# Kernel optimization log

Hardware: AMD Instinct MI355X
Metric: run time of the kernel (lower is better)

The kernel has to match this reference:

```python
import jax, jax.numpy as jnp
import numpy as np

B, NX, NLQ = 2, 2048, 64
D_IN, D_OUT, H = 768, 768, 12
HD = D_OUT // H  # 64
P_X, P_LQ = 0.1, 0.2  # dropout probs for x-x block vs any learnable-query block
DROP_KEY = 42  # fixed key for dropout masks (training mode)


def setup_inputs() -> dict:
    key = jax.random.key(0)
    ks = jax.random.split(key, 6)
    s = 0.02
    return {
        "x": jax.random.normal(ks[0], (B, NX, D_IN), jnp.float32),
        "learnable_queries": jax.random.normal(ks[1], (B, NLQ, D_IN), jnp.float32),
        "Wq": jax.random.normal(ks[2], (D_IN, D_OUT), jnp.float32) * s,
        "Wk": jax.random.normal(ks[3], (D_IN, D_OUT), jnp.float32) * s,
        "Wv": jax.random.normal(ks[4], (D_IN, D_OUT), jnp.float32) * s,
        "Wo": jax.random.normal(ks[5], (D_OUT, D_OUT), jnp.float32) * s,
        "bo": jnp.zeros((D_OUT,), jnp.float32),
    }


def reference(x, learnable_queries, Wq, Wk, Wv, Wo, bo):
    b, nx, _ = x.shape
    nlq = learnable_queries.shape[1]
    T = nx + nlq
    inp = jnp.concatenate([x, learnable_queries], axis=1)  # [b, T, d_in]

    def to_heads(W):
        return (inp @ W).reshape(b, T, H, HD).transpose(0, 2, 1, 3)  # [b, H, T, hd]

    q, k, v = to_heads(Wq), to_heads(Wk), to_heads(Wv)

    scores = jnp.einsum('bhqd,bhkd->bhqk', q, k) / np.float32(np.sqrt(HD))
    w = jax.nn.softmax(scores, axis=-1)  # [b, H, T, T]

    # --- block-structured dropout (training mode) ---
    kp_x = 1.0 - P_X
    kp_lq = 1.0 - P_LQ
    is_x = jnp.arange(T) < nx
    # keep prob is kp_x on the x-x block, kp_lq on the three lq-involving blocks
    keep_p = jnp.where(is_x[:, None] & is_x[None, :], kp_x, kp_lq)  # [T, T]
    u = jax.random.uniform(jax.random.key(DROP_KEY), (b, H, T, T), jnp.float32)
    mask = (u < keep_p).astype(w.dtype)
    n_xx = nx * nx
    n_lq_total = T * T - n_xx
    scale = (T * T) / (n_xx * kp_x + n_lq_total * kp_lq)
    w = w * mask * jnp.asarray(scale, w.dtype)

    ctx = jnp.einsum('bhqk,bhkd->bhqd', w, v)           # [b, H, T, hd]
    ctx = ctx.transpose(0, 2, 1, 3).reshape(b, T, D_OUT)  # [b, T, d_out]
    return ctx @ Wo + bo
```

## Files before the change

kernel.cpp:

```cpp
#include <hip/hip_runtime.h>
#include <stdint.h>

#define B_ 2
#define NX_ 2048
#define NLQ_ 64
#define T_ 2112
#define DIN_ 768
#define DOUT_ 768
#define NH_ 12
#define HD_ 64

#define QSZ_ ((size_t)3244032)
#define HALF_U 53526528u
#define SCALE_ ((float)(4460544.0 / (4194304.0 * 0.9 + 266240.0 * 0.8)))
#define KXS_ 3865470464u
#define KLQS_ 3435974144u

typedef __attribute__((ext_vector_type(8))) short bf16x8;
typedef __attribute__((ext_vector_type(4))) float f32x4;
typedef unsigned int uint32;

__device__ __forceinline__ uint32 rotl_(uint32 x, uint32 r) {
  return (x << r) | (x >> (32u - r));
}

__device__ __forceinline__ uint2 threefry_(uint32 x0, uint32 x1) {
  const uint32 ks0 = 0u, ks1 = 42u;
  const uint32 ks2 = 0x1BD11BDAu ^ ks0 ^ ks1;
  x0 += ks0; x1 += ks1;
#define TFR_(r) { x0 += x1; x1 = rotl_(x1, (r)); x1 ^= x0; }
  TFR_(13) TFR_(15) TFR_(26) TFR_(6)
  x0 += ks1; x1 += ks2 + 1u;
  TFR_(17) TFR_(29) TFR_(16) TFR_(24)
  x0 += ks2; x1 += ks0 + 2u;
  TFR_(13) TFR_(15) TFR_(26) TFR_(6)
  x0 += ks0; x1 += ks1 + 3u;
  TFR_(17) TFR_(29) TFR_(16) TFR_(24)
  x0 += ks1; x1 += ks2 + 4u;
  TFR_(13) TFR_(15) TFR_(26) TFR_(6)
  x0 += ks2; x1 += ks0 + 5u;
#undef TFR_
  return make_uint2(x0, x1);
}

__device__ __forceinline__ unsigned short f2b_(float f) {
  const uint32 u = __float_as_uint(f);
  return (unsigned short)((u + 0x7FFFu + ((u >> 16) & 1u)) >> 16);
}
__device__ __forceinline__ uint32 pack2_(float lo, float hi) {
  return (uint32)f2b_(lo) | ((uint32)f2b_(hi) << 16);
}

__global__ __launch_bounds__(256) void xconv_kernel(
    const float* __restrict__ xg, const float* __restrict__ lqg,
    unsigned short* __restrict__ Xb) {
  const uint32 f = (blockIdx.x * 256u + threadIdx.x) * 8u;
  const uint32 m = f / 768u;
  const uint32 col = f - m * 768u;
  const uint32 bb = (m >= (uint32)T_) ? 1u : 0u;
  const uint32 tt = m - bb * (uint32)T_;
  const float* src = (tt < NX_) ? (xg + ((size_t)bb * NX_ + tt) * DIN_ + col)
                                : (lqg + ((size_t)bb * NLQ_ + (tt - NX_)) * DIN_ + col);
  const float4 a = *(const float4*)(src);
  const float4 b = *(const float4*)(src + 4);
  uint4 o;
  o.x = pack2_(a.x, a.y); o.y = pack2_(a.z, a.w);
  o.z = pack2_(b.x, b.y); o.w = pack2_(b.z, b.w);
  *(uint4*)(Xb + f) = o;
}

__global__ __launch_bounds__(256) void prep_kernel(
    const float* __restrict__ Wq, const float* __restrict__ Wk,
    const float* __restrict__ Wv, const float* __restrict__ Wo,
    unsigned short* __restrict__ Wt) {
  __shared__ float Tf[64][65];
  const int tid = threadIdx.x;
  const int k0 = blockIdx.x << 6;
  const int n0 = blockIdx.y << 6;
  const int mat = blockIdx.z;
  const float* Wm = (mat == 0) ? Wq : (mat == 1) ? Wk : (mat == 2) ? Wv : Wo;
  const int r = tid >> 2;
  const int cch = (tid & 3) << 4;
  const float* src = Wm + (size_t)(k0 + r) * DOUT_ + n0 + cch;
#pragma unroll
  for (int j = 0; j < 4; ++j) {
    const float4 v = *(const float4*)(src + 4 * j);
    Tf[r][cch + 4 * j + 0] = v.x; Tf[r][cch + 4 * j + 1] = v.y;
    Tf[r][cch + 4 * j + 2] = v.z; Tf[r][cch + 4 * j + 3] = v.w;
  }
  __syncthreads();
  float f[16];
#pragma unroll
  for (int j = 0; j < 16; ++j) f[j] = Tf[cch + j][r];
  uint4 o0, o1;
  o0.x = pack2_(f[0], f[1]);  o0.y = pack2_(f[2], f[3]);
  o0.z = pack2_(f[4], f[5]);  o0.w = pack2_(f[6], f[7]);
  o1.x = pack2_(f[8], f[9]);  o1.y = pack2_(f[10], f[11]);
  o1.z = pack2_(f[12], f[13]); o1.w = pack2_(f[14], f[15]);
  unsigned short* dst = Wt + ((size_t)mat * DOUT_ + n0 + r) * DIN_ + k0 + cch;
  *(uint4*)dst = o0;
  *(uint4*)(dst + 8) = o1;
}

__global__ __launch_bounds__(256) void qkv_kernel(
    const unsigned short* __restrict__ Xb, const unsigned short* __restrict__ Wt,
    unsigned short* __restrict__ Qh, unsigned short* __restrict__ Kh,
    unsigned short* __restrict__ Vth, uint32* __restrict__ Mask) {
  __shared__ unsigned short AsB[4096];
  __shared__ unsigned short BsB[4096];
  const int tid = threadIdx.x;
  const int w = tid >> 6;
  const int lane = tid & 63;
  const int c = lane & 15;
  const int g = lane >> 4;
  const int wsel = blockIdx.x / NH_;
  const int h = blockIdx.x % NH_;
  const int m0 = blockIdx.y << 6;

  const int ar = tid >> 2;
  const int kpart = (tid & 3) << 4;
  const unsigned short* arow = Xb + (size_t)(m0 + ar) * DIN_;
  const unsigned short* brow = Wt + ((size_t)wsel * DOUT_ + h * HD_ + ar) * DIN_;
  const int wrA = ar * 128;
  const int swzS = (ar & 7) << 4;
  const int swzF = (c & 7) << 4;

  f32x4 ac0 = {0.f, 0.f, 0.f, 0.f}, ac1 = ac0, ac2 = ac0, ac3 = ac0;

  for (int k0 = 0; k0 < DIN_; k0 += 64) {
    const uint4 a01 = *(const uint4*)(arow + k0 + kpart);
    const uint4 a23 = *(const uint4*)(arow + k0 + kpart + 8);
    const uint4 b01 = *(const uint4*)(brow + k0 + kpart);
    const uint4 b23 = *(const uint4*)(brow + k0 + kpart + 8);
    __syncthreads();
    *(uint4*)((char*)AsB + wrA + ((kpart * 2) ^ swzS)) = a01;
    *(uint4*)((char*)AsB + wrA + ((kpart * 2 + 16) ^ swzS)) = a23;
    *(uint4*)((char*)BsB + wrA + ((kpart * 2) ^ swzS)) = b01;
    *(uint4*)((char*)BsB + wrA + ((kpart * 2 + 16) ^ swzS)) = b23;
    __syncthreads();
#pragma unroll
    for (int s = 0; s < 2; ++s) {
      const int off = ((s << 6) | (g << 4)) ^ swzF;
      const bf16x8 af = *(const bf16x8*)((const char*)AsB + (16 * w + c) * 128 + off);
      const bf16x8 b0 = *(const bf16x8*)((const char*)BsB + (c) * 128 + off);
      const bf16x8 b1 = *(const bf16x8*)((const char*)BsB + (c + 16) * 128 + off);
      const bf16x8 b2 = *(const bf16x8*)((const char*)BsB + (c + 32) * 128 + off);
      const bf16x8 b3 = *(const bf16x8*)((const char*)BsB + (c + 48) * 128 + off);
      ac0 = __builtin_amdgcn_mfma_f32_16x16x32_bf16(af, b0, ac0, 0, 0, 0);
      ac1 = __builtin_amdgcn_mfma_f32_16x16x32_bf16(af, b1, ac1, 0, 0, 0);
      ac2 = __builtin_amdgcn_mfma_f32_16x16x32_bf16(af, b2, ac2, 0, 0, 0);
      ac3 = __builtin_amdgcn_mfma_f32_16x16x32_bf16(af, b3, ac3, 0, 0, 0);
    }
  }

  const int bb2 = m0 / T_;
  const int tb = m0 - bb2 * T_;
  const size_t rowBase = (size_t)(bb2 * NH_ + h) * T_;
  if (wsel == 0) {
#pragma unroll
    for (int i = 0; i < 4; ++i) {
      const size_t rr = (rowBase + tb + 16 * w + 4 * g + i) * HD_ + c;
      Qh[rr +  0] = f2b_(ac0[i] * 0.125f);
      Qh[rr + 16] = f2b_(ac1[i] * 0.125f);
      Qh[rr + 32] = f2b_(ac2[i] * 0.125f);
      Qh[rr + 48] = f2b_(ac3[i] * 0.125f);
    }
  } else if (wsel == 1) {
#pragma unroll
    for (int i = 0; i < 4; ++i) {
      const size_t rr = (rowBase + tb + 16 * w + 4 * g + i) * HD_ + c;
      Kh[rr +  0] = f2b_(ac0[i]);
      Kh[rr + 16] = f2b_(ac1[i]);
      Kh[rr + 32] = f2b_(ac2[i]);
      Kh[rr + 48] = f2b_(ac3[i]);
    }
  } else {
    __syncthreads();
#pragma unroll
    for (int i = 0; i < 4; ++i) {
      const int col2 = (16 * w + 4 * g + i) * 2;
      *(unsigned short*)((char*)AsB + (c)      * 128 + (col2 ^ ((c & 7) << 4))) = f2b_(ac0[i]);
      *(unsigned short*)((char*)AsB + (c + 16) * 128 + (col2 ^ ((c & 7) << 4))) = f2b_(ac1[i]);
      *(unsigned short*)((char*)AsB + (c + 32) * 128 + (col2 ^ ((c & 7) << 4))) = f2b_(ac2[i]);
      *(unsigned short*)((char*)AsB + (c + 48) * 128 + (col2 ^ ((c & 7) << 4))) = f2b_(ac3[i]);
    }
    __syncthreads();
    const int hd = tid >> 2;
    const int tch = (tid & 3) << 4;
    const uint4 v0 = *(const uint4*)((const char*)AsB + hd * 128 + ((tch * 2) ^ ((hd & 7) << 4)));
    const uint4 v1 = *(const uint4*)((const char*)AsB + hd * 128 + ((tch * 2 + 16) ^ ((hd & 7) << 4)));
    unsigned short* dst = Vth + ((size_t)(bb2 * NH_ + h) * HD_ + hd) * T_ + tb + tch;
    *(uint4*)dst = v0;
    *(uint4*)(dst + 8) = v1;
  }

  const uint32 bid = (uint32)(blockIdx.y * 36 + blockIdx.x);
  const uint32 wbeg = bid * 1408u;
  for (uint32 wI = wbeg + (uint32)tid; wI < wbeg + 1408u; wI += 256u) {
    const uint32 row = wI / 66u;
    const uint32 jw  = wI - row * 66u;
    const uint32 iQ  = row % (uint32)T_;
    const uint32 thrS = (iQ < (uint32)NX_ && jw < 64u) ? KXS_ : KLQS_;
    const uint32 c0 = wI * 32u;
    uint32 word = 0u;
#pragma unroll 8
    for (int k = 0; k < 32; ++k) {
      const uint2 y = threefry_(0u, c0 + (uint32)k);
      word |= ((y.x ^ y.y) < thrS ? 1u : 0u) << k;
    }
    Mask[wI] = word;
  }
}

__global__ __launch_bounds__(256) void attn_kernel(
    const unsigned short* __restrict__ Qh, const unsigned short* __restrict__ Kh,
    const unsigned short* __restrict__ Vth, const uint32* __restrict__ Mask,
    unsigned short* __restrict__ ctx) {
  __shared__ unsigned short KsU[4096];
  __shared__ unsigned short VsU[4096];
  __shared__ unsigned short PsU[4 * 1152];
  const int tid = threadIdx.x;
  const int w = tid >> 6;
  const int lane = tid & 63;
  const int c = lane & 15;
  const int g = lane >> 4;
  const int q0 = blockIdx.x << 6;
  const int h = blockIdx.y;
  const int b = blockIdx.z;
  const size_t hbT = (size_t)(b * NH_ + h) * T_;
  const size_t vbase = (size_t)(b * NH_ + h) * HD_;

  bf16x8 aq0, aq1;
  {
    const unsigned short* qrow = Qh + (hbT + q0 + 16 * w + c) * HD_ + (g << 3);
    aq0 = *(const bf16x8*)(qrow);
    aq1 = *(const bf16x8*)(qrow + 32);
  }
  f32x4 ca0 = {0.f, 0.f, 0.f, 0.f}, ca1 = ca0, ca2 = ca0, ca3 = ca0;
  float lacc[4] = {0.f, 0.f, 0.f, 0.f};
  uint32 wb[4];
#pragma unroll
  for (int i = 0; i < 4; ++i)
    wb[i] = ((uint32)b * HALF_U +
             (uint32)(h * T_ + q0 + 16 * w + 4 * g + i) * (uint32)T_) >> 5;

  const int psE = w * 1152;
  const int psB = w * 2304;
  const int swz = (c & 7) << 4;

  for (int kt = 0; kt < T_; kt += 64) {
#pragma unroll
    for (int ii = 0; ii < 2; ++ii) {
      const int seg = tid + (ii << 8);
      const int srow = seg >> 3;
      const int sc = (seg & 7) << 3;
      const uint4 kv4 = *(const uint4*)(Kh + (hbT + kt + srow) * HD_ + sc);
      *(uint4*)((char*)KsU + srow * 128 + ((sc * 2) ^ ((srow & 7) << 4))) = kv4;
      const uint4 vv4 = *(const uint4*)(Vth + (vbase + srow) * T_ + kt + sc);
      *(uint4*)((char*)VsU + srow * 128 + ((sc * 2) ^ ((srow & 7) << 4))) = vv4;
    }
    __syncthreads();

    f32x4 sa0 = {0.f, 0.f, 0.f, 0.f}, sa1 = sa0, sa2 = sa0, sa3 = sa0;
#pragma unroll
    for (int s = 0; s < 2; ++s) {
      const int off = ((s << 6) | (g << 4)) ^ swz;
      const bf16x8 bk0 = *(const bf16x8*)((const char*)KsU + (c) * 128 + off);
      const bf16x8 bk1 = *(const bf16x8*)((const char*)KsU + (c + 16) * 128 + off);
      const bf16x8 bk2 = *(const bf16x8*)((const char*)KsU + (c + 32) * 128 + off);
      const bf16x8 bk3 = *(const bf16x8*)((const char*)KsU + (c + 48) * 128 + off);
      const bf16x8 aqs = s ? aq1 : aq0;
      sa0 = __builtin_amdgcn_mfma_f32_16x16x32_bf16(aqs, bk0, sa0, 0, 0, 0);
      sa1 = __builtin_amdgcn_mfma_f32_16x16x32_bf16(aqs, bk1, sa1, 0, 0, 0);
      sa2 = __builtin_amdgcn_mfma_f32_16x16x32_bf16(aqs, bk2, sa2, 0, 0, 0);
      sa3 = __builtin_amdgcn_mfma_f32_16x16x32_bf16(aqs, bk3, sa3, 0, 0, 0);
    }

    const uint32 ktw = (uint32)(kt >> 5);
#pragma unroll
    for (int n = 0; n < 4; ++n) {
      const f32x4 sv = (n == 0) ? sa0 : (n == 1) ? sa1 : (n == 2) ? sa2 : sa3;
      const int sh = ((n & 1) << 4) + c;
      const uint32 wOff = ktw + (n >> 1);
#pragma unroll
      for (int i = 0; i < 4; ++i) {
        const float pe = __expf(sv[i]);
        lacc[i] += pe;
        const uint32 word = Mask[wb[i] + wOff];
        PsU[psE + (4 * g + i) * 72 + 16 * n + c] =
            ((word >> sh) & 1u) ? f2b_(pe) : (unsigned short)0;
      }
    }
    __syncthreads();

    const bf16x8 ap0 = *(const bf16x8*)((const char*)PsU + psB + c * 144 + (g << 4));
    const bf16x8 ap1 = *(const bf16x8*)((const char*)PsU + psB + c * 144 + 64 + (g << 4));
#pragma unroll
    for (int s = 0; s < 2; ++s) {
      const int off = ((s << 6) | (g << 4)) ^ swz;
      const bf16x8 bv0 = *(const bf16x8*)((const char*)VsU + (c) * 128 + off);
      const bf16x8 bv1 = *(const bf16x8*)((const char*)VsU + (c + 16) * 128 + off);
      const bf16x8 bv2 = *(const bf16x8*)((const char*)VsU + (c + 32) * 128 + off);
      const bf16x8 bv3 = *(const bf16x8*)((const char*)VsU + (c + 48) * 128 + off);
      const bf16x8 aps = s ? ap1 : ap0;
      ca0 = __builtin_amdgcn_mfma_f32_16x16x32_bf16(aps, bv0, ca0, 0, 0, 0);
      ca1 = __builtin_amdgcn_mfma_f32_16x16x32_bf16(aps, bv1, ca1, 0, 0, 0);
      ca2 = __builtin_amdgcn_mfma_f32_16x16x32_bf16(aps, bv2, ca2, 0, 0, 0);
      ca3 = __builtin_amdgcn_mfma_f32_16x16x32_bf16(aps, bv3, ca3, 0, 0, 0);
    }
    __syncthreads();
  }

#pragma unroll
  for (int i = 0; i < 4; ++i) {
    float li = lacc[i];
    li += __shfl_xor(li, 1);
    li += __shfl_xor(li, 2);
    li += __shfl_xor(li, 4);
    li += __shfl_xor(li, 8);
    const float inv = SCALE_ / li;
    unsigned short* dst =
        ctx + (size_t)(b * T_ + q0 + 16 * w + 4 * g + i) * DOUT_ + (h << 6) + c;
    dst[0]  = f2b_(ca0[i] * inv);
    dst[16] = f2b_(ca1[i] * inv);
    dst[32] = f2b_(ca2[i] * inv);
    dst[48] = f2b_(ca3[i] * inv);
  }
}

__global__ __launch_bounds__(256) void oproj_kernel(
    const unsigned short* __restrict__ ctxm, const unsigned short* __restrict__ Wt,
    const float* __restrict__ bo, float* __restrict__ out) {
  __shared__ unsigned short AsB[4096];
  __shared__ unsigned short BsB[4096];
  const int tid = threadIdx.x;
  const int w = tid >> 6;
  const int lane = tid & 63;
  const int c = lane & 15;
  const int g = lane >> 4;
  const int m0 = blockIdx.x << 6;
  const int n0 = blockIdx.y << 6;
  const int ar = tid >> 2;
  const int kpart = (tid & 3) << 4;
  const unsigned short* arow = ctxm + (size_t)(m0 + ar) * DIN_;
  const unsigned short* brow = Wt + ((size_t)3 * DOUT_ + n0 + ar) * DIN_;
  const int wrA = ar * 128;
  const int swzS = (ar & 7) << 4;
  const int swzF = (c & 7) << 4;

  f32x4 ac0 = {0.f, 0.f, 0.f, 0.f}, ac1 = ac0, ac2 = ac0, ac3 = ac0;
  for (int k0 = 0; k0 < DIN_; k0 += 64) {
    const uint4 a01 = *(const uint4*)(arow + k0 + kpart);
    const uint4 a23 = *(const uint4*)(arow + k0 + kpart + 8);
    const uint4 b01 = *(const uint4*)(brow + k0 + kpart);
    const uint4 b23 = *(const uint4*)(brow + k0 + kpart + 8);
    __syncthreads();
    *(uint4*)((char*)AsB + wrA + ((kpart * 2) ^ swzS)) = a01;
    *(uint4*)((char*)AsB + wrA + ((kpart * 2 + 16) ^ swzS)) = a23;
    *(uint4*)((char*)BsB + wrA + ((kpart * 2) ^ swzS)) = b01;
    *(uint4*)((char*)BsB + wrA + ((kpart * 2 + 16) ^ swzS)) = b23;
    __syncthreads();
#pragma unroll
    for (int s = 0; s < 2; ++s) {
      const int off = ((s << 6) | (g << 4)) ^ swzF;
      const bf16x8 af = *(const bf16x8*)((const char*)AsB + (16 * w + c) * 128 + off);
      const bf16x8 b0 = *(const bf16x8*)((const char*)BsB + (c) * 128 + off);
      const bf16x8 b1 = *(const bf16x8*)((const char*)BsB + (c + 16) * 128 + off);
      const bf16x8 b2 = *(const bf16x8*)((const char*)BsB + (c + 32) * 128 + off);
      const bf16x8 b3 = *(const bf16x8*)((const char*)BsB + (c + 48) * 128 + off);
      ac0 = __builtin_amdgcn_mfma_f32_16x16x32_bf16(af, b0, ac0, 0, 0, 0);
      ac1 = __builtin_amdgcn_mfma_f32_16x16x32_bf16(af, b1, ac1, 0, 0, 0);
      ac2 = __builtin_amdgcn_mfma_f32_16x16x32_bf16(af, b2, ac2, 0, 0, 0);
      ac3 = __builtin_amdgcn_mfma_f32_16x16x32_bf16(af, b3, ac3, 0, 0, 0);
    }
  }
  const float bi0 = bo[n0 + c];
  const float bi1 = bo[n0 + 16 + c];
  const float bi2 = bo[n0 + 32 + c];
  const float bi3 = bo[n0 + 48 + c];
#pragma unroll
  for (int i = 0; i < 4; ++i) {
    float* dst = out + (size_t)(m0 + 16 * w + 4 * g + i) * DOUT_ + n0 + c;
    dst[0]  = ac0[i] + bi0;
    dst[16] = ac1[i] + bi1;
    dst[32] = ac2[i] + bi2;
    dst[48] = ac3[i] + bi3;
  }
}

extern "C" void kernel_launch(void* const* d_in, const int* in_sizes, int n_in,
                              void* d_out, int out_size, void* d_ws, size_t ws_size,
                              hipStream_t stream) {
  (void)in_sizes; (void)n_in; (void)out_size; (void)ws_size;
  const float* x  = (const float*)d_in[0];
  const float* lq = (const float*)d_in[1];
  const float* Wq = (const float*)d_in[2];
  const float* Wk = (const float*)d_in[3];
  const float* Wv = (const float*)d_in[4];
  const float* Wo = (const float*)d_in[5];
  const float* bo = (const float*)d_in[6];
  unsigned short* Qh  = (unsigned short*)d_ws;
  unsigned short* Kh  = Qh + QSZ_;
  unsigned short* Vth = Kh + QSZ_;
  unsigned short* Cb  = Vth + QSZ_;
  unsigned short* Xb  = Cb;
  unsigned short* Wt  = (unsigned short*)((char*)d_ws + 32440320);
  uint32* Mask = (uint32*)((char*)d_ws + 37158912);
  xconv_kernel<<<dim3(1584), dim3(256), 0, stream>>>(x, lq, Xb);
  prep_kernel<<<dim3(12, 12, 4), dim3(256), 0, stream>>>(Wq, Wk, Wv, Wo, Wt);
  qkv_kernel<<<dim3(36, 66), dim3(256), 0, stream>>>(Xb, Wt, Qh, Kh, Vth, Mask);
  attn_kernel<<<dim3(33, NH_, B_), dim3(256), 0, stream>>>(Qh, Kh, Vth, Mask, Cb);
  oproj_kernel<<<dim3(66, 12), dim3(256), 0, stream>>>(Cb, Wt, bo, (float*)d_out);
}
```

Before: 410.0 us.

## Double-buffer LDS tiles in QKV and attention loops with register prefetch

After: 402.6 us. About the same (-1.8%).

```diff
diff --git a/kernel.cpp b/kernel.cpp
--- a/kernel.cpp
+++ b/kernel.cpp
@@ -106,8 +106,8 @@
     const unsigned short* __restrict__ Xb, const unsigned short* __restrict__ Wt,
     unsigned short* __restrict__ Qh, unsigned short* __restrict__ Kh,
     unsigned short* __restrict__ Vth, uint32* __restrict__ Mask) {
-  __shared__ unsigned short AsB[4096];
-  __shared__ unsigned short BsB[4096];
+  __shared__ unsigned short AsB[2][4096];
+  __shared__ unsigned short BsB[2][4096];
   const int tid = threadIdx.x;
   const int w = tid >> 6;
   const int lane = tid & 63;
@@ -125,31 +125,49 @@
   const int swzS = (ar & 7) << 4;
   const int swzF = (c & 7) << 4;
 
+  {
+    const uint4 a01 = *(const uint4*)(arow + kpart);
+    const uint4 a23 = *(const uint4*)(arow + kpart + 8);
+    const uint4 b01 = *(const uint4*)(brow + kpart);
+    const uint4 b23 = *(const uint4*)(brow + kpart + 8);
+    *(uint4*)((char*)AsB[0] + wrA + ((kpart * 2) ^ swzS)) = a01;
+    *(uint4*)((char*)AsB[0] + wrA + ((kpart * 2 + 16) ^ swzS)) = a23;
+    *(uint4*)((char*)BsB[0] + wrA + ((kpart * 2) ^ swzS)) = b01;
+    *(uint4*)((char*)BsB[0] + wrA + ((kpart * 2 + 16) ^ swzS)) = b23;
+  }
+
   f32x4 ac0 = {0.f, 0.f, 0.f, 0.f}, ac1 = ac0, ac2 = ac0, ac3 = ac0;
 
-  for (int k0 = 0; k0 < DIN_; k0 += 64) {
-    const uint4 a01 = *(const uint4*)(arow + k0 + kpart);
-    const uint4 a23 = *(const uint4*)(arow + k0 + kpart + 8);
-    const uint4 b01 = *(const uint4*)(brow + k0 + kpart);
-    const uint4 b23 = *(const uint4*)(brow + k0 + kpart + 8);
-    __syncthreads();
-    *(uint4*)((char*)AsB + wrA + ((kpart * 2) ^ swzS)) = a01;
-    *(uint4*)((char*)AsB + wrA + ((kpart * 2 + 16) ^ swzS)) = a23;
-    *(uint4*)((char*)BsB + wrA + ((kpart * 2) ^ swzS)) = b01;
-    *(uint4*)((char*)BsB + wrA + ((kpart * 2 + 16) ^ swzS)) = b23;
+  for (int kt = 0; kt < 12; ++kt) {
+    const int cur = kt & 1;
+    uint4 na01, na23, nb01, nb23;
+    if (kt < 11) {
+      const int k0 = (kt + 1) << 6;
+      na01 = *(const uint4*)(arow + k0 + kpart);
+      na23 = *(const uint4*)(arow + k0 + kpart + 8);
+      nb01 = *(const uint4*)(brow + k0 + kpart);
+      nb23 = *(const uint4*)(brow + k0 + kpart + 8);
+    }
     __syncthreads();
 #pragma unroll
     for (int s = 0; s < 2; ++s) {
       const int off = ((s << 6) | (g << 4)) ^ swzF;
-      const bf16x8 af = *(const bf16x8*)((const char*)AsB + (16 * w + c) * 128 + off);
-      const bf16x8 b0 = *(const bf16x8*)((const char*)BsB + (c) * 128 + off);
-      const bf16x8 b1 = *(const bf16x8*)((const char*)BsB + (c + 16) * 128 + off);
-      const bf16x8 b2 = *(const bf16x8*)((const char*)BsB + (c + 32) * 128 + off);
-      const bf16x8 b3 = *(const bf16x8*)((const char*)BsB + (c + 48) * 128 + off);
+      const bf16x8 af = *(const bf16x8*)((const char*)AsB[cur] + (16 * w + c) * 128 + off);
+      const bf16x8 b0 = *(const bf16x8*)((const char*)BsB[cur] + (c) * 128 + off);
+      const bf16x8 b1 = *(const bf16x8*)((const char*)BsB[cur] + (c + 16) * 128 + off);
+      const bf16x8 b2 = *(const bf16x8*)((const char*)BsB[cur] + (c + 32) * 128 + off);
+      const bf16x8 b3 = *(const bf16x8*)((const char*)BsB[cur] + (c + 48) * 128 + off);
       ac0 = __builtin_amdgcn_mfma_f32_16x16x32_bf16(af, b0, ac0, 0, 0, 0);
       ac1 = __builtin_amdgcn_mfma_f32_16x16x32_bf16(af, b1, ac1, 0, 0, 0);
       ac2 = __builtin_amdgcn_mfma_f32_16x16x32_bf16(af, b2, ac2, 0, 0, 0);
       ac3 = __builtin_amdgcn_mfma_f32_16x16x32_bf16(af, b3, ac3, 0, 0, 0);
+    }
+    if (kt < 11) {
+      const int nxt = cur ^ 1;
+      *(uint4*)((char*)AsB[nxt] + wrA + ((kpart * 2) ^ swzS)) = na01;
+      *(uint4*)((char*)AsB[nxt] + wrA + ((kpart * 2 + 16) ^ swzS)) = na23;
+      *(uint4*)((char*)BsB[nxt] + wrA + ((kpart * 2) ^ swzS)) = nb01;
+      *(uint4*)((char*)BsB[nxt] + wrA + ((kpart * 2 + 16) ^ swzS)) = nb23;
     }
   }
 
@@ -175,20 +193,19 @@
       Kh[rr + 48] = f2b_(ac3[i]);
     }
   } else {
-    __syncthreads();
 #pragma unroll
     for (int i = 0; i < 4; ++i) {
       const int col2 = (16 * w + 4 * g + i) * 2;
-      *(unsigned short*)((char*)AsB + (c)      * 128 + (col2 ^ ((c & 7) << 4))) = f2b_(ac0[i]);
-      *(unsigned short*)((char*)AsB + (c + 16) * 128 + (col2 ^ ((c & 7) << 4))) = f2b_(ac1[i]);
-      *(unsigned short*)((char*)AsB + (c + 32) * 128 + (col2 ^ ((c & 7) << 4))) = f2b_(ac2[i]);
-      *(unsigned short*)((char*)AsB + (c + 48) * 128 + (col2 ^ ((c & 7) << 4))) = f2b_(ac3[i]);
+      *(unsigned short*)((char*)AsB[0] + (c)      * 128 + (col2 ^ ((c & 7) << 4))) = f2b_(ac0[i]);
+      *(unsigned short*)((char*)AsB[0] + (c + 16) * 128 + (col2 ^ ((c & 7) << 4))) = f2b_(ac1[i]);
+      *(unsigned short*)((char*)AsB[0] + (c + 32) * 128 + (col2 ^ ((c & 7) << 4))) = f2b_(ac2[i]);
+      *(unsigned short*)((char*)AsB[0] + (c + 48) * 128 + (col2 ^ ((c & 7) << 4))) = f2b_(ac3[i]);
     }
     __syncthreads();
     const int hd = tid >> 2;
     const int tch = (tid & 3) << 4;
-    const uint4 v0 = *(const uint4*)((const char*)AsB + hd * 128 + ((tch * 2) ^ ((hd & 7) << 4)));
-    const uint4 v1 = *(const uint4*)((const char*)AsB + hd * 128 + ((tch * 2 + 16) ^ ((hd & 7) << 4)));
+    const uint4 v0 = *(const uint4*)((const char*)AsB[0] + hd * 128 + ((tch * 2) ^ ((hd & 7) << 4)));
+    const uint4 v1 = *(const uint4*)((const char*)AsB[0] + hd * 128 + ((tch * 2 + 16) ^ ((hd & 7) << 4)));
     unsigned short* dst = Vth + ((size_t)(bb2 * NH_ + h) * HD_ + hd) * T_ + tb + tch;
     *(uint4*)dst = v0;
     *(uint4*)(dst + 8) = v1;
@@ -216,8 +233,8 @@
     const unsigned short* __restrict__ Qh, const unsigned short* __restrict__ Kh,
     const unsigned short* __restrict__ Vth, const uint32* __restrict__ Mask,
     unsigned short* __restrict__ ctx) {
-  __shared__ unsigned short KsU[4096];
-  __shared__ unsigned short VsU[4096];
+  __shared__ unsigned short KsU[2][4096];
+  __shared__ unsigned short VsU[2][4096];
   __shared__ unsigned short PsU[4 * 1152];
   const int tid = threadIdx.x;
   const int w = tid >> 6;
@@ -247,17 +264,32 @@
   const int psE = w * 1152;
   const int psB = w * 2304;
   const int swz = (c & 7) << 4;
-
-  for (int kt = 0; kt < T_; kt += 64) {
-#pragma unroll
-    for (int ii = 0; ii < 2; ++ii) {
-      const int seg = tid + (ii << 8);
-      const int srow = seg >> 3;
-      const int sc = (seg & 7) << 3;
-      const uint4 kv4 = *(const uint4*)(Kh + (hbT + kt + srow) * HD_ + sc);
-      *(uint4*)((char*)KsU + srow * 128 + ((sc * 2) ^ ((srow & 7) << 4))) = kv4;
-      const uint4 vv4 = *(const uint4*)(Vth + (vbase + srow) * T_ + kt + sc);
-      *(uint4*)((char*)VsU + srow * 128 + ((sc * 2) ^ ((srow & 7) << 4))) = vv4;
+  const int srow0 = tid >> 3;
+  const int sc0 = (tid & 7) << 3;
+  const int srow1 = (tid + 256) >> 3;
+  const int sc1 = ((tid + 256) & 7) << 3;
+
+  {
+    *(uint4*)((char*)KsU[0] + srow0 * 128 + ((sc0 * 2) ^ ((srow0 & 7) << 4))) =
+        *(const uint4*)(Kh + (hbT + srow0) * HD_ + sc0);
+    *(uint4*)((char*)VsU[0] + srow0 * 128 + ((sc0 * 2) ^ ((srow0 & 7) << 4))) =
+        *(const uint4*)(Vth + (vbase + srow0) * T_ + sc0);
+    *(uint4*)((char*)KsU[0] + srow1 * 128 + ((sc1 * 2) ^ ((srow1 & 7) << 4))) =
+        *(const uint4*)(Kh + (hbT + srow1) * HD_ + sc1);
+    *(uint4*)((char*)VsU[0] + srow1 * 128 + ((sc1 * 2) ^ ((srow1 & 7) << 4))) =
+        *(const uint4*)(Vth + (vbase + srow1) * T_ + sc1);
+  }
+
+  for (int t = 0; t < 33; ++t) {
+    const int cur = t & 1;
+    const int kt = t << 6;
+    uint4 nk0, nv0, nk1, nv1;
+    if (t < 32) {
+      const int ktn = kt + 64;
+      nk0 = *(const uint4*)(Kh + (hbT + ktn + srow0) * HD_ + sc0);
+      nv0 = *(const uint4*)(Vth + (vbase + srow0) * T_ + ktn + sc0);
+      nk1 = *(const uint4*)(Kh + (hbT + ktn + srow1) * HD_ + sc1);
+      nv1 = *(const uint4*)(Vth + (vbase + srow1) * T_ + ktn + sc1);
     }
     __syncthreads();
 
@@ -265,10 +297,10 @@
 #pragma unroll
     for (int s = 0; s < 2; ++s) {
       const int off = ((s << 6) | (g << 4)) ^ swz;
-      const bf16x8 bk0 = *(const bf16x8*)((const char*)KsU + (c) * 128 + off);
-      const bf16x8 bk1 = *(const bf16x8*)((const char*)KsU + (c + 16) * 128 + off);
-      const bf16x8 bk2 = *(const bf16x8*)((const char*)KsU + (c + 32) * 128 + off);
-      const bf16x8 bk3 = *(const bf16x8*)((const char*)KsU + (c + 48) * 128 + off);
+      const bf16x8 bk0 = *(const bf16x8*)((const char*)KsU[cur] + (c) * 128 + off);
+      const bf16x8 bk1 = *(const bf16x8*)((const char*)KsU[cur] + (c + 16) * 128 + off);
+      const bf16x8 bk2 = *(const bf16x8*)((const char*)KsU[cur] + (c + 32) * 128 + off);
+      const bf16x8 bk3 = *(const bf16x8*)((const char*)KsU[cur] + (c + 48) * 128 + off);
       const bf16x8 aqs = s ? aq1 : aq0;
       sa0 = __builtin_amdgcn_mfma_f32_16x16x32_bf16(aqs, bk0, sa0, 0, 0, 0);
       sa1 = __builtin_amdgcn_mfma_f32_16x16x32_bf16(aqs, bk1, sa1, 0, 0, 0);
@@ -291,24 +323,31 @@
             ((word >> sh) & 1u) ? f2b_(pe) : (unsigned short)0;
       }
     }
-    __syncthreads();
+    asm volatile("s_waitcnt lgkmcnt(0)" ::: "memory");
 
     const bf16x8 ap0 = *(const bf16x8*)((const char*)PsU + psB + c * 144 + (g << 4));
     const bf16x8 ap1 = *(const bf16x8*)((const char*)PsU + psB + c * 144 + 64 + (g << 4));
 #pragma unroll
     for (int s = 0; s < 2; ++s) {
       const int off = ((s << 6) | (g << 4)) ^ swz;
-      const bf16x8 bv0 = *(const bf16x8*)((const char*)VsU + (c) * 128 + off);
-      const bf16x8 bv1 = *(const bf16x8*)((const char*)VsU + (c + 16) * 128 + off);
-      const bf16x8 bv2 = *(const bf16x8*)((const char*)VsU + (c + 32) * 128 + off);
-      const bf16x8 bv3 = *(const bf16x8*)((const char*)VsU + (c + 48) * 128 + off);
+      const bf16x8 bv0 = *(const bf16x8*)((const char*)VsU[cur] + (c) * 128 + off);
+      const bf16x8 bv1 = *(const bf16x8*)((const char*)VsU[cur] + (c + 16) * 128 + off);
+      const bf16x8 bv2 = *(const bf16x8*)((const char*)VsU[cur] + (c + 32) * 128 + off);
+      const bf16x8 bv3 = *(const bf16x8*)((const char*)VsU[cur] + (c + 48) * 128 + off);
       const bf16x8 aps = s ? ap1 : ap0;
       ca0 = __builtin_amdgcn_mfma_f32_16x16x32_bf16(aps, bv0, ca0, 0, 0, 0);
       ca1 = __builtin_amdgcn_mfma_f32_16x16x32_bf16(aps, bv1, ca1, 0, 0, 0);
       ca2 = __builtin_amdgcn_mfma_f32_16x16x32_bf16(aps, bv2, ca2, 0, 0, 0);
       ca3 = __builtin_amdgcn_mfma_f32_16x16x32_bf16(aps, bv3, ca3, 0, 0, 0);
     }
-    __syncthreads();
+
+    if (t < 32) {
+      const int nxt = cur ^ 1;
+      *(uint4*)((char*)KsU[nxt] + srow0 * 128 + ((sc0 * 2) ^ ((srow0 & 7) << 4))) = nk0;
+      *(uint4*)((char*)VsU[nxt] + srow0 * 128 + ((sc0 * 2) ^ ((srow0 & 7) << 4))) = nv0;
+      *(uint4*)((char*)KsU[nxt] + srow1 * 128 + ((sc1 * 2) ^ ((srow1 & 7) << 4))) = nk1;
+      *(uint4*)((char*)VsU[nxt] + srow1 * 128 + ((sc1 * 2) ^ ((srow1 & 7) << 4))) = nv1;
+    }
   }
 
 #pragma unroll
```
